# Kernel tuning notes

Hardware: AMD Instinct MI355X
Metric: run time of the kernel (lower is better)

Reference implementation:

```python
import jax, jax.numpy as jnp
import numpy as np

TAU = 0.2
LW = 0.5
EPS = 1e-12  # tf.math.l2_normalize epsilon


def _l2norm(x):
    ss = jnp.sum(x * x, axis=-1, keepdims=True)
    return x * jax.lax.rsqrt(jnp.maximum(ss, EPS))


def _global_head(f, W1, b1, W2, b2):
    g = jnp.mean(f, axis=(1, 2))            # GlobalAveragePooling2D -> [B, C]
    h = jax.nn.relu(g @ W1 + b1)
    return h @ W2 + b2                      # [B, 128]


def _dense_head(f, W1, b1, W2, b2):
    # 1x1 convs == per-pixel matmuls
    h = jax.nn.relu(jnp.einsum('bhwc,cd->bhwd', f, W1) + b1)
    return jnp.einsum('bhwd,de->bhwe', h, W2) + b2  # [B, H, W, 128]


def _info_nce(q, k):
    logits = (q @ k.T) / TAU                # [N, N]
    lse = jax.nn.logsumexp(logits, axis=-1)
    pos = jnp.diagonal(logits)
    return jnp.mean(lse - pos)


def setup_inputs() -> dict:
    key = jax.random.key(0)
    ks = jax.random.split(key, 10)
    B, H, W, C = 128, 7, 7, 2048
    Dh, De = 2048, 128
    s1 = 1.0 / np.sqrt(C)
    s2 = 1.0 / np.sqrt(Dh)
    inp = {
        'feat_q': jax.random.normal(ks[0], (B, H, W, C), jnp.float32),
        'feat_k': jax.random.normal(ks[1], (B, H, W, C), jnp.float32),
        'Wg1': jax.random.normal(ks[2], (C, Dh), jnp.float32) * s1,
        'bg1': jnp.zeros((Dh,), jnp.float32),
        'Wg2': jax.random.normal(ks[3], (Dh, De), jnp.float32) * s2,
        'bg2': jnp.zeros((De,), jnp.float32),
        'Wd1': jax.random.normal(ks[4], (C, Dh), jnp.float32) * s1,
        'bd1': jnp.zeros((Dh,), jnp.float32),
        'Wd2': jax.random.normal(ks[5], (Dh, De), jnp.float32) * s2,
        'bd2': jnp.zeros((De,), jnp.float32),
        'mWg1': jax.random.normal(ks[6], (C, Dh), jnp.float32) * s1,
        'mbg1': jnp.zeros((Dh,), jnp.float32),
        'mWg2': jax.random.normal(ks[7], (Dh, De), jnp.float32) * s2,
        'mbg2': jnp.zeros((De,), jnp.float32),
        'mWd1': jax.random.normal(ks[8], (C, Dh), jnp.float32) * s1,
        'mbd1': jnp.zeros((Dh,), jnp.float32),
        'mWd2': jax.random.normal(ks[9], (Dh, De), jnp.float32) * s2,
        'mbd2': jnp.zeros((De,), jnp.float32),
    }
    return inp


def reference(feat_q, feat_k, Wg1, bg1, Wg2, bg2, Wd1, bd1, Wd2, bd2,
              mWg1, mbg1, mWg2, mbg2, mWd1, mbd1, mWd2, mbd2):
    # query (student) branch
    q_g = _l2norm(_global_head(feat_q, Wg1, bg1, Wg2, bg2))      # [B, 128]
    q_d = _l2norm(_dense_head(feat_q, Wd1, bd1, Wd2, bd2))       # [B, H, W, 128]
    # key (momentum teacher) branch, stop-gradient as in train_step
    k_g = jax.lax.stop_gradient(_l2norm(_global_head(feat_k, mWg1, mbg1, mWg2, mbg2)))
    k_d = jax.lax.stop_gradient(_l2norm(_dense_head(feat_k, mWd1, mbd1, mWd2, mbd2)))

    l_g = _info_nce(q_g, k_g)

    B, H, W, De = q_d.shape
    f1 = q_d.reshape(B, H * W, De)
    f2 = k_d.reshape(B, H * W, De)
    sim = jnp.einsum('bnc,bmc->bnm', f1, f2)                     # [B, HW, HW]
    idx = jnp.argmax(sim, axis=-1)                               # [B, HW]
    matched = jnp.take_along_axis(f2, idx[..., None], axis=1)    # [B, HW, 128]

    l_d = _info_nce(f1.reshape(-1, De), matched.reshape(-1, De))
    total = (1.0 - LW) * l_g + LW * l_d
    return total
```

## Files before the change

kernel.cpp:

```cpp
#include <hip/hip_runtime.h>
#include <cstddef>

typedef __bf16 bf16x8 __attribute__((ext_vector_type(8)));
typedef float  f32x4  __attribute__((ext_vector_type(4)));
typedef unsigned short u16x8 __attribute__((ext_vector_type(8)));

__device__ __forceinline__ float b2f(unsigned short u) {
    union { unsigned int i; float f; } v; v.i = ((unsigned int)u) << 16; return v.f;
}
__device__ __forceinline__ unsigned short f2b(float f) {
    union { float f; unsigned int i; } v; v.f = f;
    unsigned int r = v.i + 0x7fffu + ((v.i >> 16) & 1u);
    return (unsigned short)(r >> 16);
}
__device__ __forceinline__ void gl_lds16(const void* g, void* l) {
    __builtin_amdgcn_global_load_lds((const __attribute__((address_space(1))) void*)g,
                                     (__attribute__((address_space(3))) void*)l,
                                     16, 0, 0);
}

__global__ __launch_bounds__(64) void detect_kernel(const unsigned short* __restrict__ feat,
                                                    int* __restrict__ flag) {
    __shared__ int cnt;
    if (threadIdx.x == 0) cnt = 0;
    __syncthreads();
    int c = 0;
    for (int i = threadIdx.x; i < 256; i += 64) {
        float v = b2f(feat[i]);
        if (fabsf(v) > 100.0f) ++c;
    }
    atomicAdd(&cnt, c);
    __syncthreads();
    if (threadIdx.x == 0) *flag = (cnt > 16) ? 1 : 0;
}

__global__ __launch_bounds__(256) void zero_kernel(float* __restrict__ p, int n4) {
    int i = blockIdx.x * 256 + threadIdx.x;
    const f32x4 z = {0.f, 0.f, 0.f, 0.f};
    if (i < n4) ((f32x4*)p)[i] = z;
}

__global__ __launch_bounds__(256) void convpool_kernel(const void* __restrict__ fq,
                                                       const void* __restrict__ fk,
                                                       unsigned short* __restrict__ FQ,
                                                       unsigned short* __restrict__ FK,
                                                       unsigned short* __restrict__ gq,
                                                       unsigned short* __restrict__ gk,
                                                       const int* __restrict__ flagp) {
    int fl = *flagp;
    int b = blockIdx.y;
    const void* src = blockIdx.z ? fk : fq;
    unsigned short* dst = blockIdx.z ? FK : FQ;
    unsigned short* g   = blockIdx.z ? gk : gq;
    int c0 = threadIdx.x * 8;
    float s[8];
    #pragma unroll
    for (int j = 0; j < 8; ++j) s[j] = 0.f;
    for (int p = 0; p < 49; ++p) {
        size_t idx = ((size_t)b * 49 + p) * 2048 + c0;
        u16x8 o;
        if (fl) {
            const float* sf = (const float*)src + idx;
            f32x4 v0 = *(const f32x4*)sf;
            f32x4 v1 = *(const f32x4*)(sf + 4);
            o[0]=f2b(v0[0]); o[1]=f2b(v0[1]); o[2]=f2b(v0[2]); o[3]=f2b(v0[3]);
            o[4]=f2b(v1[0]); o[5]=f2b(v1[1]); o[6]=f2b(v1[2]); o[7]=f2b(v1[3]);
            s[0]+=v0[0]; s[1]+=v0[1]; s[2]+=v0[2]; s[3]+=v0[3];
            s[4]+=v1[0]; s[5]+=v1[1]; s[6]+=v1[2]; s[7]+=v1[3];
        } else {
            o = *(const u16x8*)((const unsigned short*)src + idx);
            #pragma unroll
            for (int j = 0; j < 8; ++j) s[j] += b2f(o[j]);
        }
        *(u16x8*)(dst + idx) = o;
    }
    u16x8 gm;
    #pragma unroll
    for (int j = 0; j < 8; ++j) gm[j] = f2b(s[j] * (1.0f / 49.0f));
    *(u16x8*)(g + (size_t)b * 2048 + c0) = gm;
}

__global__ __launch_bounds__(256) void convert_kernel(const void* __restrict__ in,
                                                      unsigned short* __restrict__ out,
                                                      const int* __restrict__ flagp) {
    int fl = *flagp;
    size_t i = ((size_t)blockIdx.x * 256 + threadIdx.x) * 8;
    if (fl) {
        const float* inf = (const float*)in;
        f32x4 v0 = *(const f32x4*)(inf + i);
        f32x4 v1 = *(const f32x4*)(inf + i + 4);
        u16x8 o;
        o[0]=f2b(v0[0]); o[1]=f2b(v0[1]); o[2]=f2b(v0[2]); o[3]=f2b(v0[3]);
        o[4]=f2b(v1[0]); o[5]=f2b(v1[1]); o[6]=f2b(v1[2]); o[7]=f2b(v1[3]);
        *(u16x8*)(out + i) = o;
    } else {
        *(u16x8*)(out + i) = *(const u16x8*)((const unsigned short*)in + i);
    }
}

__global__ __launch_bounds__(256) void pool_kernel(const void* __restrict__ fq,
                                                   const void* __restrict__ fk,
                                                   unsigned short* __restrict__ gq,
                                                   unsigned short* __restrict__ gk,
                                                   const int* __restrict__ flagp) {
    int fl = *flagp;
    int c = blockIdx.x * 256 + threadIdx.x;
    int b = blockIdx.y;
    const void* src = blockIdx.z ? fk : fq;
    unsigned short* dst = blockIdx.z ? gk : gq;
    size_t base = (size_t)b * 49 * 2048 + c;
    float s = 0.f;
    if (fl) {
        const float* sf = (const float*)src;
        #pragma unroll
        for (int p = 0; p < 49; ++p) s += sf[base + (size_t)p * 2048];
    } else {
        const unsigned short* su = (const unsigned short*)src;
        #pragma unroll
        for (int p = 0; p < 49; ++p) s += b2f(su[base + (size_t)p * 2048]);
    }
    dst[(size_t)b * 2048 + c] = f2b(s * (1.0f / 49.0f));
}

__global__ __launch_bounds__(256) void transpose2v_kernel(
    const void* __restrict__ s0, const void* __restrict__ s1,
    unsigned short* __restrict__ d0, unsigned short* __restrict__ d1,
    int rows, int cols, const int* __restrict__ flagp) {
    int fl = *flagp;
    int z = blockIdx.z;
    const void* in = z ? s1 : s0;
    unsigned short* out = z ? d1 : d0;
    __shared__ unsigned short tile[64 * 72];
    int bx = blockIdx.x * 64, by = blockIdx.y * 64;
    int tr = threadIdx.x >> 3;
    int tc = (threadIdx.x & 7) * 8;
    #pragma unroll
    for (int h = 0; h < 2; ++h) {
        int r = tr + h * 32;
        if (fl) {
            const float* inf = (const float*)in + (size_t)(by + r) * cols + bx + tc;
            f32x4 v0 = *(const f32x4*)inf;
            f32x4 v1 = *(const f32x4*)(inf + 4);
            u16x8 o;
            o[0]=f2b(v0[0]); o[1]=f2b(v0[1]); o[2]=f2b(v0[2]); o[3]=f2b(v0[3]);
            o[4]=f2b(v1[0]); o[5]=f2b(v1[1]); o[6]=f2b(v1[2]); o[7]=f2b(v1[3]);
            *(u16x8*)(tile + r * 72 + tc) = o;
        } else {
            const unsigned short* inu = (const unsigned short*)in + (size_t)(by + r) * cols + bx + tc;
            *(u16x8*)(tile + r * 72 + tc) = *(const u16x8*)inu;
        }
    }
    __syncthreads();
    #pragma unroll
    for (int h = 0; h < 2; ++h) {
        int oc = tr + h * 32;
        u16x8 v;
        #pragma unroll
        for (int j = 0; j < 8; ++j) v[j] = tile[(tc + j) * 72 + oc];
        *(u16x8*)(out + (size_t)(bx + oc) * rows + by + tc) = v;
    }
}

__global__ __launch_bounds__(256) void transpose4v_kernel(
    const void* __restrict__ s0, const void* __restrict__ s1,
    const void* __restrict__ s2, const void* __restrict__ s3,
    unsigned short* __restrict__ d0, unsigned short* __restrict__ d1,
    unsigned short* __restrict__ d2, unsigned short* __restrict__ d3,
    int rows, int cols, const int* __restrict__ flagp) {
    int fl = *flagp;
    int z = blockIdx.z;
    const void* in = (z == 0) ? s0 : (z == 1) ? s1 : (z == 2) ? s2 : s3;
    unsigned short* out = (z == 0) ? d0 : (z == 1) ? d1 : (z == 2) ? d2 : d3;
    __shared__ unsigned short tile[64 * 72];
    int bx = blockIdx.x * 64, by = blockIdx.y * 64;
    int tr = threadIdx.x >> 3;
    int tc = (threadIdx.x & 7) * 8;
    #pragma unroll
    for (int h = 0; h < 2; ++h) {
        int r = tr + h * 32;
        if (fl) {
            const float* inf = (const float*)in + (size_t)(by + r) * cols + bx + tc;
            f32x4 v0 = *(const f32x4*)inf;
            f32x4 v1 = *(const f32x4*)(inf + 4);
            u16x8 o;
            o[0]=f2b(v0[0]); o[1]=f2b(v0[1]); o[2]=f2b(v0[2]); o[3]=f2b(v0[3]);
            o[4]=f2b(v1[0]); o[5]=f2b(v1[1]); o[6]=f2b(v1[2]); o[7]=f2b(v1[3]);
            *(u16x8*)(tile + r * 72 + tc) = o;
        } else {
            const unsigned short* inu = (const unsigned short*)in + (size_t)(by + r) * cols + bx + tc;
            *(u16x8*)(tile + r * 72 + tc) = *(const u16x8*)inu;
        }
    }
    __syncthreads();
    #pragma unroll
    for (int h = 0; h < 2; ++h) {
        int oc = tr + h * 32;
        u16x8 v;
        #pragma unroll
        for (int j = 0; j < 8; ++j) v[j] = tile[(tc + j) * 72 + oc];
        *(u16x8*)(out + (size_t)(bx + oc) * rows + by + tc) = v;
    }
}

__device__ __forceinline__ void mlp_body(
    const unsigned short* __restrict__ A, const unsigned short* __restrict__ Bt,
    const unsigned short* __restrict__ W2, const void* __restrict__ b1,
    float* __restrict__ outp, size_t m0, size_t n0, int fl)
{
    const int K = 2048;
    __shared__ unsigned short smem[8192 + 9216];
    unsigned short* As = smem;
    unsigned short* Bs = smem + 8192;
    unsigned short* Hs = smem + 8192;

    int tid  = threadIdx.x;
    int lane = tid & 63;
    int w    = tid >> 6;
    int wm = w & 1, wn = w >> 1;
    int quad = lane >> 4, l16 = lane & 15;
    int lrow = lane >> 3;
    int kc   = (lane & 7) ^ lrow;

    const unsigned short* gA[4];
    const unsigned short* gB[4];
    unsigned short* lA[4];
    unsigned short* lB[4];
    #pragma unroll
    for (int c = 0; c < 4; ++c) {
        int row = w * 32 + c * 8 + lrow;
        gA[c] = A  + (m0 + row) * (size_t)K + kc * 8;
        gB[c] = Bt + (n0 + row) * (size_t)K + kc * 8;
        lA[c] = As + w * 2048 + c * 512;
        lB[c] = Bs + w * 2048 + c * 512;
    }

    const f32x4 zero4 = {0.f, 0.f, 0.f, 0.f};
    f32x4 acc[4][4];
    #pragma unroll
    for (int i = 0; i < 4; ++i)
        #pragma unroll
        for (int j = 0; j < 4; ++j) acc[i][j] = zero4;

    int swz = l16 & 7;
    for (int kb = 0; kb < K / 64; ++kb) {
        __syncthreads();
        #pragma unroll
        for (int c = 0; c < 4; ++c) { gl_lds16(gA[c], lA[c]); gA[c] += 64; }
        #pragma unroll
        for (int c = 0; c < 4; ++c) { gl_lds16(gB[c], lB[c]); gB[c] += 64; }
        __syncthreads();
        #pragma unroll
        for (int k0 = 0; k0 < 64; k0 += 32) {
            bf16x8 af[4], bfr[4];
            #pragma unroll
            for (int mt = 0; mt < 4; ++mt) {
                int row = wm * 64 + mt * 16 + l16;
                int sc  = (((k0 >> 3) + quad) ^ swz) << 3;
                af[mt] = *(const bf16x8*)(As + row * 64 + sc);
            }
            #pragma unroll
            for (int nt = 0; nt < 4; ++nt) {
                int row = wn * 64 + nt * 16 + l16;
                int sc  = (((k0 >> 3) + quad) ^ swz) << 3;
                bfr[nt] = *(const bf16x8*)(Bs + row * 64 + sc);
            }
            #pragma unroll
            for (int mt = 0; mt < 4; ++mt)
                #pragma unroll
                for (int nt = 0; nt < 4; ++nt)
                    acc[mt][nt] = __builtin_amdgcn_mfma_f32_16x16x32_bf16(af[mt], bfr[nt], acc[mt][nt], 0, 0, 0);
        }
    }

    float b1v[4];
    #pragma unroll
    for (int nt = 0; nt < 4; ++nt) {
        int col = (int)n0 + wn * 64 + nt * 16 + l16;
        b1v[nt] = fl ? ((const float*)b1)[col] : b2f(((const unsigned short*)b1)[col]);
    }

    f32x4 acc2[4][4];
    #pragma unroll
    for (int i = 0; i < 4; ++i)
        #pragma unroll
        for (int j = 0; j < 4; ++j) acc2[i][j] = zero4;

    #pragma unroll
    for (int hf = 0; hf < 2; ++hf) {
        __syncthreads();
        if (wn == hf) {
            #pragma unroll
            for (int mt = 0; mt < 4; ++mt)
                #pragma unroll
                for (int nt = 0; nt < 4; ++nt)
                    #pragma unroll
                    for (int r = 0; r < 4; ++r) {
                        float v = fmaxf(acc[mt][nt][r] + b1v[nt], 0.f);
                        Hs[(wm * 64 + mt * 16 + quad * 4 + r) * 72 + nt * 16 + l16] = f2b(v);
                    }
        } else {
            #pragma unroll
            for (int c = 0; c < 8; ++c) {
                const unsigned short* g = W2 + (size_t)(wm * 64 + c * 8 + lrow) * 2048
                                          + n0 + hf * 64 + kc * 8;
                gl_lds16(g, As + wm * 4096 + c * 512);
            }
        }
        __syncthreads();
        #pragma unroll
        for (int k0 = 0; k0 < 64; k0 += 32) {
            bf16x8 ha[4], wb[4];
            #pragma unroll
            for (int mt = 0; mt < 4; ++mt)
                ha[mt] = *(const bf16x8*)(Hs + (wm * 64 + mt * 16 + l16) * 72 + k0 + quad * 8);
            #pragma unroll
            for (int et = 0; et < 4; ++et) {
                int row = wn * 64 + et * 16 + l16;
                int sc  = (((k0 >> 3) + quad) ^ swz) << 3;
                wb[et] = *(const bf16x8*)(As + row * 64 + sc);
            }
            #pragma unroll
            for (int mt = 0; mt < 4; ++mt)
                #pragma unroll
                for (int et = 0; et < 4; ++et)
                    acc2[mt][et] = __builtin_amdgcn_mfma_f32_16x16x32_bf16(ha[mt], wb[et], acc2[mt][et], 0, 0, 0);
        }
    }

    #pragma unroll
    for (int et = 0; et < 4; ++et) {
        int col = wn * 64 + et * 16 + l16;
        #pragma unroll
        for (int mt = 0; mt < 4; ++mt)
            #pragma unroll
            for (int r = 0; r < 4; ++r) {
                size_t row = m0 + wm * 64 + mt * 16 + quad * 4 + r;
                atomicAdd(&outp[row * 128 + col], acc2[mt][et][r]);
            }
    }
}

__global__ __launch_bounds__(256) void mlp_mega_kernel(
    const unsigned short* __restrict__ FQ, const unsigned short* __restrict__ FK,
    const unsigned short* __restrict__ gq, const unsigned short* __restrict__ gk,
    const unsigned short* __restrict__ WD1T, const unsigned short* __restrict__ MWD1T,
    const unsigned short* __restrict__ WG1T, const unsigned short* __restrict__ MWG1T,
    const unsigned short* __restrict__ W2dq, const unsigned short* __restrict__ W2dk,
    const unsigned short* __restrict__ W2gq, const unsigned short* __restrict__ W2gk,
    const void* __restrict__ bd1, const void* __restrict__ mbd1,
    const void* __restrict__ bg1, const void* __restrict__ mbg1,
    float* __restrict__ rawdq, float* __restrict__ rawdk,
    float* __restrict__ rawgq, float* __restrict__ rawgk,
    const int* __restrict__ flagp)
{
    int fl = *flagp;
    int z = blockIdx.z;
    int isg = (blockIdx.y == 49);
    const unsigned short *A, *Bt, *W2; const void* b1; float* outp;
    if (!isg) {
        A = z ? FK : FQ;  Bt = z ? MWD1T : WD1T;  W2 = z ? W2dk : W2dq;
        b1 = z ? mbd1 : bd1;  outp = z ? rawdk : rawdq;
    } else {
        A = z ? gk : gq;  Bt = z ? MWG1T : WG1T;  W2 = z ? W2gk : W2gq;
        b1 = z ? mbg1 : bg1;  outp = z ? rawgk : rawgq;
    }
    size_t m0 = isg ? 0 : (size_t)blockIdx.y * 128;
    size_t n0 = (size_t)blockIdx.x * 128;
    mlp_body(A, Bt, W2, b1, outp, m0, n0, fl);
}

__global__ __launch_bounds__(256) void mlp_kernel(
    const unsigned short* __restrict__ A0, const unsigned short* __restrict__ A1,
    const unsigned short* __restrict__ Bt0, const unsigned short* __restrict__ Bt1,
    const unsigned short* __restrict__ W20, const unsigned short* __restrict__ W21,
    const void* __restrict__ b10, const void* __restrict__ b11,
    float* __restrict__ out0, float* __restrict__ out1,
    const int* __restrict__ flagp)
{
    int fl = *flagp;
    int z  = blockIdx.z;
    mlp_body(z ? A1 : A0, z ? Bt1 : Bt0, z ? W21 : W20, z ? b11 : b10,
             z ? out1 : out0, (size_t)blockIdx.y * 128, (size_t)blockIdx.x * 128, fl);
}

__global__ __launch_bounds__(256) void simmatch_kernel(
    const float* __restrict__ rawdq, const float* __restrict__ rawdk,
    const void* __restrict__ bd2, const void* __restrict__ mbd2,
    unsigned short* __restrict__ qd, unsigned short* __restrict__ kd,
    unsigned short* __restrict__ matched, float* __restrict__ pos,
    const int* __restrict__ flagp) {
    int fl = *flagp;
    __shared__ float f1s[49 * 128];
    __shared__ float f2s[49 * 128];
    int b = blockIdx.x;
    int t = threadIdx.x;
    size_t base = (size_t)b * 49 * 128;

    int rr = t >> 2, jq = t & 3;
    if (rr < 49) {
        #pragma unroll
        for (int br = 0; br < 2; ++br) {
            const float* raw = br ? rawdk : rawdq;
            const void* bias = br ? mbd2 : bd2;
            unsigned short* outg = br ? kd : qd;
            float* fs = br ? f2s : f1s;
            size_t idx = base + (size_t)rr * 128 + jq * 32;
            float x[32];
            float ss = 0.f;
            #pragma unroll
            for (int c = 0; c < 32; ++c) {
                float bv = fl ? ((const float*)bias)[jq * 32 + c]
                              : b2f(((const unsigned short*)bias)[jq * 32 + c]);
                x[c] = raw[idx + c] + bv;
                ss += x[c] * x[c];
            }
            ss += __shfl_xor(ss, 1); ss += __shfl_xor(ss, 2);
            float rs = rsqrtf(fmaxf(ss, 1e-12f));
            #pragma unroll
            for (int c = 0; c < 32; ++c) {
                unsigned short us = f2b(x[c] * rs);
                outg[idx + c] = us;
                fs[rr * 128 + jq * 32 + c] = b2f(us);
            }
        }
    }
    __syncthreads();

    int i = t >> 2, q4 = t & 3;
    if (i < 49) {
        int mlo = q4 * 13;
        int mhi = mlo + 13; if (mhi > 49) mhi = 49;
        float best = -1e30f; int bi = 1 << 20;
        const f32x4* va = (const f32x4*)(f1s + i * 128);
        for (int m = mlo; m < mhi; ++m) {
            const f32x4* vb = (const f32x4*)(f2s + m * 128);
            float d = 0.f;
            #pragma unroll
            for (int j = 0; j < 32; ++j) {
                f32x4 a = va[j], bb = vb[j];
                d += a[0]*bb[0] + a[1]*bb[1] + a[2]*bb[2] + a[3]*bb[3];
            }
            if (d > best) { best = d; bi = m; }
        }
        #pragma unroll
        for (int off = 1; off < 4; off <<= 1) {
            float ov = __shfl_xor(best, off);
            int   oi = __shfl_xor(bi, off);
            if (ov > best || (ov == best && oi < bi)) { best = ov; bi = oi; }
        }
        if (q4 == 0) pos[b * 49 + i] = best * 5.0f;
        for (int j = q4 * 32; j < q4 * 32 + 32; ++j)
            matched[base + (size_t)i * 128 + j] = f2b(f2s[bi * 128 + j]);
    }
}

#define KS 136
__global__ __launch_bounds__(256) void lse_kernel(const unsigned short* __restrict__ qd,
                                                  const unsigned short* __restrict__ matched,
                                                  float* __restrict__ lsep) {
    __shared__ unsigned short As[128 * KS];
    __shared__ unsigned short Bs[64 * KS];
    __shared__ float rsum[128];
    int tid  = threadIdx.x;
    int lane = tid & 63, wave = tid >> 6;
    int wm = wave & 1, wn = wave >> 1;
    int quad = lane >> 4, l16 = lane & 15;
    size_t m0 = (size_t)blockIdx.x * 128;
    int z = blockIdx.y;

    #pragma unroll
    for (int i = 0; i < 8; ++i) {
        int l = tid + 256 * i;
        int row = l >> 4, ko = (l & 15) << 3;
        u16x8 v = *(const u16x8*)(qd + (m0 + row) * 128 + ko);
        *(u16x8*)(As + row * KS + ko) = v;
    }
    if (tid < 128) rsum[tid] = 0.f;

    float rs[4][4];
    #pragma unroll
    for (int mt = 0; mt < 4; ++mt)
        #pragma unroll
        for (int r = 0; r < 4; ++r) rs[mt][r] = 0.f;

    const f32x4 zero4 = {0.f, 0.f, 0.f, 0.f};
    int nlo = z * 896, nhi = nlo + 896;
    for (int n0 = nlo; n0 < nhi; n0 += 64) {
        __syncthreads();
        #pragma unroll
        for (int i = 0; i < 4; ++i) {
            int l = tid + 256 * i;
            int row = l >> 4, ko = (l & 15) << 3;
            u16x8 v = *(const u16x8*)(matched + (size_t)(n0 + row) * 128 + ko);
            *(u16x8*)(Bs + row * KS + ko) = v;
        }
        __syncthreads();
        f32x4 acc[4][2];
        #pragma unroll
        for (int mt = 0; mt < 4; ++mt) { acc[mt][0] = zero4; acc[mt][1] = zero4; }
        #pragma unroll
        for (int k0 = 0; k0 < 128; k0 += 32) {
            bf16x8 af[4], bfr[2];
            #pragma unroll
            for (int mt = 0; mt < 4; ++mt)
                af[mt] = *(const bf16x8*)(As + (wm * 64 + mt * 16 + l16) * KS + k0 + quad * 8);
            #pragma unroll
            for (int nt = 0; nt < 2; ++nt)
                bfr[nt] = *(const bf16x8*)(Bs + (wn * 32 + nt * 16 + l16) * KS + k0 + quad * 8);
            #pragma unroll
            for (int mt = 0; mt < 4; ++mt)
                #pragma unroll
                for (int nt = 0; nt < 2; ++nt)
                    acc[mt][nt] = __builtin_amdgcn_mfma_f32_16x16x32_bf16(af[mt], bfr[nt], acc[mt][nt], 0, 0, 0);
        }
        #pragma unroll
        for (int mt = 0; mt < 4; ++mt)
            #pragma unroll
            for (int r = 0; r < 4; ++r)
                rs[mt][r] += __expf(acc[mt][0][r] * 5.0f) + __expf(acc[mt][1][r] * 5.0f);
    }
    #pragma unroll
    for (int mt = 0; mt < 4; ++mt)
        #pragma unroll
        for (int r = 0; r < 4; ++r) {
            float v = rs[mt][r];
            v += __shfl_xor(v, 1); v += __shfl_xor(v, 2);
            v += __shfl_xor(v, 4); v += __shfl_xor(v, 8);
            if (l16 == 0) atomicAdd(&rsum[wm * 64 + mt * 16 + quad * 4 + r], v);
        }
    __syncthreads();
    if (tid < 128) lsep[(size_t)z * 6272 + m0 + tid] = rsum[tid];
}

__global__ __launch_bounds__(128) void lg_kernel(const float* __restrict__ rawgq,
                                                 const float* __restrict__ rawgk,
                                                 const void* __restrict__ bg2,
                                                 const void* __restrict__ mbg2,
                                                 float* __restrict__ lgrow,
                                                 const int* __restrict__ flagp) {
    int fl = *flagp;
    __shared__ float ksf[128 * 128];
    __shared__ float qsf[8 * 128];
    int t = threadIdx.x;
    int rbase = blockIdx.x * 8;
    {
        const float* rk = rawgk + (size_t)t * 128;
        float ss = 0.f;
        for (int c = 0; c < 128; ++c) {
            float bv = fl ? ((const float*)mbg2)[c] : b2f(((const unsigned short*)mbg2)[c]);
            float xx = rk[c] + bv;
            ss += xx * xx;
        }
        float rsv = rsqrtf(fmaxf(ss, 1e-12f));
        for (int c = 0; c < 128; ++c) {
            float bv = fl ? ((const float*)mbg2)[c] : b2f(((const unsigned short*)mbg2)[c]);
            ksf[t * 128 + c] = b2f(f2b((rk[c] + bv) * rsv));
        }
    }
    if (t < 8) {
        const float* rq = rawgq + (size_t)(rbase + t) * 128;
        float ss = 0.f;
        for (int c = 0; c < 128; ++c) {
            float bv = fl ? ((const float*)bg2)[c] : b2f(((const unsigned short*)bg2)[c]);
            float xx = rq[c] + bv;
            ss += xx * xx;
        }
        float rsv = rsqrtf(fmaxf(ss, 1e-12f));
        for (int c = 0; c < 128; ++c) {
            float bv = fl ? ((const float*)bg2)[c] : b2f(((const unsigned short*)bg2)[c]);
            qsf[t * 128 + c] = b2f(f2b((rq[c] + bv) * rsv));
        }
    }
    __syncthreads();
    int rl = t >> 4, jg = t & 15;
    int row = rbase + rl;
    float se = 0.f, diag = 0.f;
    for (int jj = 0; jj < 8; ++jj) {
        int j = jg * 8 + jj;
        float d = 0.f;
        #pragma unroll 8
        for (int c = 0; c < 128; ++c) d += qsf[rl * 128 + c] * ksf[j * 128 + c];
        d *= 5.0f;
        se += __expf(d);
        if (j == row) diag = d;
    }
    #pragma unroll
    for (int off = 1; off < 16; off <<= 1) { se += __shfl_xor(se, off); diag += __shfl_xor(diag, off); }
    if (jg == 0) lgrow[row] = logf(se) - diag;
}

__global__ __launch_bounds__(256) void final_kernel(const float* __restrict__ lsep,
                                                    const float* __restrict__ pos,
                                                    const float* __restrict__ lgrow,
                                                    unsigned int* __restrict__ out) {
    int t = threadIdx.x;
    float s = 0.f;
    for (int i = t; i < 6272; i += 256) {
        float se = 0.f;
        #pragma unroll
        for (int zz = 0; zz < 7; ++zz) se += lsep[zz * 6272 + i];
        s += logf(se) - pos[i];
    }
    float g = (t < 128) ? lgrow[t] : 0.f;
    #pragma unroll
    for (int off = 32; off >= 1; off >>= 1) { s += __shfl_xor(s, off); g += __shfl_xor(g, off); }
    __shared__ float p8[8];
    if ((t & 63) == 0) { p8[t >> 6] = s; p8[4 + (t >> 6)] = g; }
    __syncthreads();
    if (t == 0) {
        float ld  = (p8[0] + p8[1] + p8[2] + p8[3]) * (1.0f / 6272.0f);
        float lg  = (p8[4] + p8[5] + p8[6] + p8[7]) * (1.0f / 128.0f);
        float total = 0.5f * lg + 0.5f * ld;
        unsigned int L = f2b(total);
        union { float f; unsigned int u; } tb; tb.f = total;
        unsigned int base = (tb.u & 0xFFFF0000u) | L;
        unsigned int bu = base; float be = 1e30f;
        #pragma unroll
        for (int d = -1; d <= 1; ++d) {
            unsigned int c = base + ((unsigned int)d << 16);
            union { unsigned int u; float f; } cv; cv.u = c;
            float e = fabsf(cv.f - total);
            if (e < be) { be = e; bu = c; }
        }
        out[0] = bu;
    }
}

#define A_FQ     ((size_t)0)
#define A_FK     ((size_t)25690112)
#define A_WD1T   ((size_t)51380224)
#define A_MWD1T  ((size_t)59768832)
#define A_WG1T   ((size_t)68157440)
#define A_MWG1T  ((size_t)76546048)
#define A_W2DQ   ((size_t)84934656)
#define A_W2DK   ((size_t)85458944)
#define A_W2GQ   ((size_t)85983232)
#define A_W2GK   ((size_t)86507520)
#define A_RAWDQ  ((size_t)87031808)
#define A_RAWDK  ((size_t)90243072)
#define A_RAWGQ  ((size_t)93454336)
#define A_RAWGK  ((size_t)93519872)
#define A_GQ     ((size_t)93585408)
#define A_GK     ((size_t)94109696)
#define A_QD     ((size_t)94633984)
#define A_KD     ((size_t)96239616)
#define A_MT     ((size_t)97845248)
#define A_POS    ((size_t)99450880)
#define A_LSEP   ((size_t)99475968)
#define A_LGR    ((size_t)99651584)
#define A_FLAG   ((size_t)99652096)
#define A_NEED   ((size_t)99652608)

#define B_SLOTA  ((size_t)0)
#define B_QD     ((size_t)0)
#define B_KD     ((size_t)1605632)
#define B_MT     ((size_t)3211264)
#define B_SLOTB  ((size_t)8388608)
#define B_W2DQ   ((size_t)34078720)
#define B_W2DK   ((size_t)34603008)
#define B_W2GQ   ((size_t)35127296)
#define B_W2GK   ((size_t)35651584)
#define B_RAWDQ  ((size_t)36175872)
#define B_RAWDK  ((size_t)39387136)
#define B_RAWGQ  ((size_t)42598400)
#define B_RAWGK  ((size_t)42663936)
#define B_GQ     ((size_t)42729472)
#define B_GK     ((size_t)43253760)
#define B_POS    ((size_t)42729472)
#define B_LSEP   ((size_t)42754560)
#define B_LGR    ((size_t)42930176)
#define B_FLAG   ((size_t)42930688)

extern "C" void kernel_launch(void* const* d_in, const int* in_sizes, int n_in,
                              void* d_out, int out_size, void* d_ws, size_t ws_size,
                              hipStream_t stream) {
    (void)in_sizes; (void)n_in; (void)out_size;
    const void* feat_q = d_in[0];
    const void* feat_k = d_in[1];
    const void* Wg1 = d_in[2];  const void* bg1 = d_in[3];
    const void* Wg2 = d_in[4];  const void* bg2 = d_in[5];
    const void* Wd1 = d_in[6];  const void* bd1 = d_in[7];
    const void* Wd2 = d_in[8];  const void* bd2 = d_in[9];
    const void* mWg1 = d_in[10]; const void* mbg1 = d_in[11];
    const void* mWg2 = d_in[12]; const void* mbg2 = d_in[13];
    const void* mWd1 = d_in[14]; const void* mbd1 = d_in[15];
    const void* mWd2 = d_in[16]; const void* mbd2 = d_in[17];
    char* ws = (char*)d_ws;

    if (ws_size >= A_NEED) {
        unsigned short* FQ    = (unsigned short*)(ws + A_FQ);
        unsigned short* FK    = (unsigned short*)(ws + A_FK);
        unsigned short* WD1T  = (unsigned short*)(ws + A_WD1T);
        unsigned short* MWD1T = (unsigned short*)(ws + A_MWD1T);
        unsigned short* WG1T  = (unsigned short*)(ws + A_WG1T);
        unsigned short* MWG1T = (unsigned short*)(ws + A_MWG1T);
        unsigned short* W2dq  = (unsigned short*)(ws + A_W2DQ);
        unsigned short* W2dk  = (unsigned short*)(ws + A_W2DK);
        unsigned short* W2gq  = (unsigned short*)(ws + A_W2GQ);
        unsigned short* W2gk  = (unsigned short*)(ws + A_W2GK);
        float* rawdq = (float*)(ws + A_RAWDQ);
        float* rawdk = (float*)(ws + A_RAWDK);
        float* rawgq = (float*)(ws + A_RAWGQ);
        float* rawgk = (float*)(ws + A_RAWGK);
        unsigned short* gq = (unsigned short*)(ws + A_GQ);
        unsigned short* gk = (unsigned short*)(ws + A_GK);
        unsigned short* qd = (unsigned short*)(ws + A_QD);
        unsigned short* kd = (unsigned short*)(ws + A_KD);
        unsigned short* mt = (unsigned short*)(ws + A_MT);
        float* pos  = (float*)(ws + A_POS);
        float* lsep = (float*)(ws + A_LSEP);
        float* lgr  = (float*)(ws + A_LGR);
        int*   flag = (int*)(ws + A_FLAG);

        detect_kernel<<<1, 64, 0, stream>>>((const unsigned short*)feat_q, flag);
        convpool_kernel<<<dim3(1, 128, 2), 256, 0, stream>>>(feat_q, feat_k, FQ, FK, gq, gk, flag);
        transpose4v_kernel<<<dim3(32, 32, 4), 256, 0, stream>>>(
            Wd1, mWd1, Wg1, mWg1, WD1T, MWD1T, WG1T, MWG1T, 2048, 2048, flag);
        transpose4v_kernel<<<dim3(2, 32, 4), 256, 0, stream>>>(
            Wd2, mWd2, Wg2, mWg2, W2dq, W2dk, W2gq, W2gk, 2048, 128, flag);
        zero_kernel<<<1600, 256, 0, stream>>>(rawdq, 409600);
        mlp_mega_kernel<<<dim3(16, 50, 2), 256, 0, stream>>>(
            FQ, FK, gq, gk, WD1T, MWD1T, WG1T, MWG1T,
            W2dq, W2dk, W2gq, W2gk, bd1, mbd1, bg1, mbg1,
            rawdq, rawdk, rawgq, rawgk, flag);
        simmatch_kernel<<<128, 256, 0, stream>>>(rawdq, rawdk, bd2, mbd2, qd, kd, mt, pos, flag);
        lse_kernel<<<dim3(49, 7), 256, 0, stream>>>(qd, mt, lsep);
        lg_kernel<<<16, 128, 0, stream>>>(rawgq, rawgk, bg2, mbg2, lgr, flag);
        final_kernel<<<1, 256, 0, stream>>>(lsep, pos, lgr, (unsigned int*)d_out);
    } else {
        unsigned short* slotA = (unsigned short*)(ws + B_SLOTA);
        unsigned short* slotB = (unsigned short*)(ws + B_SLOTB);
        unsigned short* W2dq = (unsigned short*)(ws + B_W2DQ);
        unsigned short* W2dk = (unsigned short*)(ws + B_W2DK);
        unsigned short* W2gq = (unsigned short*)(ws + B_W2GQ);
        unsigned short* W2gk = (unsigned short*)(ws + B_W2GK);
        float* rawdq = (float*)(ws + B_RAWDQ);
        float* rawdk = (float*)(ws + B_RAWDK);
        float* rawgq = (float*)(ws + B_RAWGQ);
        float* rawgk = (float*)(ws + B_RAWGK);
        unsigned short* gq = (unsigned short*)(ws + B_GQ);
        unsigned short* gk = (unsigned short*)(ws + B_GK);
        unsigned short* qd = (unsigned short*)(ws + B_QD);
        unsigned short* kd = (unsigned short*)(ws + B_KD);
        unsigned short* mt = (unsigned short*)(ws + B_MT);
        float* pos  = (float*)(ws + B_POS);
        float* lsep = (float*)(ws + B_LSEP);
        float* lgr  = (float*)(ws + B_LGR);
        int*   flag = (int*)(ws + B_FLAG);

        detect_kernel<<<1, 64, 0, stream>>>((const unsigned short*)feat_q, flag);
        pool_kernel<<<dim3(8, 128, 2), 256, 0, stream>>>(feat_q, feat_k, gq, gk, flag);
        transpose2v_kernel<<<dim3(32, 32, 2), 256, 0, stream>>>(Wg1, mWg1, slotA, slotB, 2048, 2048, flag);
        transpose4v_kernel<<<dim3(2, 32, 4), 256, 0, stream>>>(
            Wd2, mWd2, Wg2, mWg2, W2dq, W2dk, W2gq, W2gk, 2048, 128, flag);
        zero_kernel<<<1600, 256, 0, stream>>>(rawdq, 409600);
        mlp_kernel<<<dim3(16, 1, 2), 256, 0, stream>>>(
            gq, gk, slotA, slotB, W2gq, W2gk, bg1, mbg1, rawgq, rawgk, flag);
        transpose2v_kernel<<<dim3(32, 32, 1), 256, 0, stream>>>(Wd1, Wd1, slotA, slotA, 2048, 2048, flag);
        convert_kernel<<<6272, 256, 0, stream>>>(feat_q, slotB, flag);
        mlp_kernel<<<dim3(16, 49, 1), 256, 0, stream>>>(
            slotB, slotB, slotA, slotA, W2dq, W2dq, bd1, bd1, rawdq, rawdq, flag);
        transpose2v_kernel<<<dim3(32, 32, 1), 256, 0, stream>>>(mWd1, mWd1, slotA, slotA, 2048, 2048, flag);
        convert_kernel<<<6272, 256, 0, stream>>>(feat_k, slotB, flag);
        mlp_kernel<<<dim3(16, 49, 1), 256, 0, stream>>>(
            slotB, slotB, slotA, slotA, W2dk, W2dk, mbd1, mbd1, rawdk, rawdk, flag);
        simmatch_kernel<<<128, 256, 0, stream>>>(rawdq, rawdk, bd2, mbd2, qd, kd, mt, pos, flag);
        lse_kernel<<<dim3(49, 7), 256, 0, stream>>>(qd, mt, lsep);
        lg_kernel<<<16, 128, 0, stream>>>(rawgq, rawgk, bg2, mbg2, lgr, flag);
        final_kernel<<<1, 256, 0, stream>>>(lsep, pos, lgr, (unsigned int*)d_out);
    }
}
```

Baseline: 571.6 us.

## Double-buffer MLP GEMM LDS tiles, add XCD block swizzle, widen convpool grid

The MLP GEMM main loop now uses two LDS buffers, so the global-to-LDS loads for the next K-slice are issued while MFMAs run on the current one. This halves the barriers per K step. The mlp kernels also remap block indices so that neighbouring tiles land on the same XCD, which should improve L2 reuse of the shared weight and activation panels. The convpool kernel is split across twice as many blocks with 4-wide vectors to add parallelism. In exchange, LDS use grows to 64KB per block, which may lower occupancy.

```diff
diff --git a/kernel.cpp b/kernel.cpp
--- a/kernel.cpp
+++ b/kernel.cpp
@@ -4,6 +4,7 @@
 typedef __bf16 bf16x8 __attribute__((ext_vector_type(8)));
 typedef float  f32x4  __attribute__((ext_vector_type(4)));
 typedef unsigned short u16x8 __attribute__((ext_vector_type(8)));
+typedef unsigned short u16x4 __attribute__((ext_vector_type(4)));
 
 __device__ __forceinline__ float b2f(unsigned short u) {
     union { unsigned int i; float f; } v; v.i = ((unsigned int)u) << 16; return v.f;
@@ -17,6 +18,19 @@
     __builtin_amdgcn_global_load_lds((const __attribute__((address_space(1))) void*)g,
                                      (__attribute__((address_space(3))) void*)l,
                                      16, 0, 0);
+}
+
+__device__ __forceinline__ void xcd_swizzle(int& bx, int& by, int& bz) {
+    unsigned int nx = gridDim.x, ny = gridDim.y;
+    unsigned int n = nx * ny * gridDim.z;
+    unsigned int lin = blockIdx.x + nx * (blockIdx.y + ny * blockIdx.z);
+    unsigned int q = n >> 3, r = n & 7u;
+    unsigned int xcd = lin & 7u, off = lin >> 3;
+    unsigned int s = (xcd < r) ? (xcd * (q + 1u) + off)
+                               : (r * (q + 1u) + (xcd - r) * q + off);
+    bx = (int)(s % nx); s /= nx;
+    by = (int)(s % ny);
+    bz = (int)(s / ny);
 }
 
 __global__ __launch_bounds__(64) void detect_kernel(const unsigned short* __restrict__ feat,
@@ -52,32 +66,28 @@
     const void* src = blockIdx.z ? fk : fq;
     unsigned short* dst = blockIdx.z ? FK : FQ;
     unsigned short* g   = blockIdx.z ? gk : gq;
-    int c0 = threadIdx.x * 8;
-    float s[8];
-    #pragma unroll
-    for (int j = 0; j < 8; ++j) s[j] = 0.f;
+    int c0 = blockIdx.x * 1024 + threadIdx.x * 4;
+    float s[4];
+    #pragma unroll
+    for (int j = 0; j < 4; ++j) s[j] = 0.f;
     for (int p = 0; p < 49; ++p) {
         size_t idx = ((size_t)b * 49 + p) * 2048 + c0;
-        u16x8 o;
+        u16x4 o;
         if (fl) {
-            const float* sf = (const float*)src + idx;
-            f32x4 v0 = *(const f32x4*)sf;
-            f32x4 v1 = *(const f32x4*)(sf + 4);
-            o[0]=f2b(v0[0]); o[1]=f2b(v0[1]); o[2]=f2b(v0[2]); o[3]=f2b(v0[3]);
-            o[4]=f2b(v1[0]); o[5]=f2b(v1[1]); o[6]=f2b(v1[2]); o[7]=f2b(v1[3]);
-            s[0]+=v0[0]; s[1]+=v0[1]; s[2]+=v0[2]; s[3]+=v0[3];
-            s[4]+=v1[0]; s[5]+=v1[1]; s[6]+=v1[2]; s[7]+=v1[3];
+            f32x4 v = *(const f32x4*)((const float*)src + idx);
+            o[0]=f2b(v[0]); o[1]=f2b(v[1]); o[2]=f2b(v[2]); o[3]=f2b(v[3]);
+            s[0]+=v[0]; s[1]+=v[1]; s[2]+=v[2]; s[3]+=v[3];
         } else {
-            o = *(const u16x8*)((const unsigned short*)src + idx);
-            #pragma unroll
-            for (int j = 0; j < 8; ++j) s[j] += b2f(o[j]);
-        }
-        *(u16x8*)(dst + idx) = o;
-    }
-    u16x8 gm;
-    #pragma unroll
-    for (int j = 0; j < 8; ++j) gm[j] = f2b(s[j] * (1.0f / 49.0f));
-    *(u16x8*)(g + (size_t)b * 2048 + c0) = gm;
+            o = *(const u16x4*)((const unsigned short*)src + idx);
+            #pragma unroll
+            for (int j = 0; j < 4; ++j) s[j] += b2f(o[j]);
+        }
+        *(u16x4*)(dst + idx) = o;
+    }
+    u16x4 gm;
+    #pragma unroll
+    for (int j = 0; j < 4; ++j) gm[j] = f2b(s[j] * (1.0f / 49.0f));
+    *(u16x4*)(g + (size_t)b * 2048 + c0) = gm;
 }
 
 __global__ __launch_bounds__(256) void convert_kernel(const void* __restrict__ in,
@@ -208,10 +218,13 @@
     float* __restrict__ outp, size_t m0, size_t n0, int fl)
 {
     const int K = 2048;
-    __shared__ unsigned short smem[8192 + 9216];
-    unsigned short* As = smem;
-    unsigned short* Bs = smem + 8192;
-    unsigned short* Hs = smem + 8192;
+    __shared__ unsigned short smem[32768];
+    unsigned short* As0 = smem;
+    unsigned short* Bs0 = smem + 8192;
+    unsigned short* As1 = smem + 16384;
+    unsigned short* Bs1 = smem + 24576;
+    unsigned short* W2s = smem;
+    unsigned short* Hs  = smem + 8192;
 
     int tid  = threadIdx.x;
     int lane = tid & 63;
@@ -223,15 +236,13 @@
 
     const unsigned short* gA[4];
     const unsigned short* gB[4];
-    unsigned short* lA[4];
-    unsigned short* lB[4];
+    int off[4];
     #pragma unroll
     for (int c = 0; c < 4; ++c) {
         int row = w * 32 + c * 8 + lrow;
         gA[c] = A  + (m0 + row) * (size_t)K + kc * 8;
         gB[c] = Bt + (n0 + row) * (size_t)K + kc * 8;
-        lA[c] = As + w * 2048 + c * 512;
-        lB[c] = Bs + w * 2048 + c * 512;
+        off[c] = w * 2048 + c * 512;
     }
 
     const f32x4 zero4 = {0.f, 0.f, 0.f, 0.f};
@@ -242,35 +253,51 @@
         for (int j = 0; j < 4; ++j) acc[i][j] = zero4;
 
     int swz = l16 & 7;
-    for (int kb = 0; kb < K / 64; ++kb) {
+
+#define STAGE(Ad, Bd) do { \
+    _Pragma("unroll") \
+    for (int c = 0; c < 4; ++c) { gl_lds16(gA[c], (Ad) + off[c]); gA[c] += 64; } \
+    _Pragma("unroll") \
+    for (int c = 0; c < 4; ++c) { gl_lds16(gB[c], (Bd) + off[c]); gB[c] += 64; } \
+} while (0)
+
+#define CSTEP(Asrc, Bsrc) do { \
+    _Pragma("unroll") \
+    for (int k0 = 0; k0 < 64; k0 += 32) { \
+        bf16x8 af[4], bfr[4]; \
+        _Pragma("unroll") \
+        for (int mt = 0; mt < 4; ++mt) { \
+            int row = wm * 64 + mt * 16 + l16; \
+            int sc  = (((k0 >> 3) + quad) ^ swz) << 3; \
+            af[mt] = *(const bf16x8*)((Asrc) + row * 64 + sc); \
+        } \
+        _Pragma("unroll") \
+        for (int nt = 0; nt < 4; ++nt) { \
+            int row = wn * 64 + nt * 16 + l16; \
+            int sc  = (((k0 >> 3) + quad) ^ swz) << 3; \
+            bfr[nt] = *(const bf16x8*)((Bsrc) + row * 64 + sc); \
+        } \
+        _Pragma("unroll") \
+        for (int mt = 0; mt < 4; ++mt) \
+            _Pragma("unroll") \
+            for (int nt = 0; nt < 4; ++nt) \
+                acc[mt][nt] = __builtin_amdgcn_mfma_f32_16x16x32_bf16(af[mt], bfr[nt], acc[mt][nt], 0, 0, 0); \
+    } \
+} while (0)
+
+    STAGE(As0, Bs0);
+    __syncthreads();
+    #pragma unroll 1
+    for (int kb2 = 0; kb2 < 16; ++kb2) {
+        STAGE(As1, Bs1);
+        CSTEP(As0, Bs0);
         __syncthreads();
-        #pragma unroll
-        for (int c = 0; c < 4; ++c) { gl_lds16(gA[c], lA[c]); gA[c] += 64; }
-        #pragma unroll
-        for (int c = 0; c < 4; ++c) { gl_lds16(gB[c], lB[c]); gB[c] += 64; }
+        if (kb2 < 15) STAGE(As0, Bs0);
+        CSTEP(As1, Bs1);
         __syncthreads();
-        #pragma unroll
-        for (int k0 = 0; k0 < 64; k0 += 32) {
-            bf16x8 af[4], bfr[4];
-            #pragma unroll
-            for (int mt = 0; mt < 4; ++mt) {
-                int row = wm * 64 + mt * 16 + l16;
-                int sc  = (((k0 >> 3) + quad) ^ swz) << 3;
-                af[mt] = *(const bf16x8*)(As + row * 64 + sc);
-            }
-            #pragma unroll
-            for (int nt = 0; nt < 4; ++nt) {
-                int row = wn * 64 + nt * 16 + l16;
-                int sc  = (((k0 >> 3) + quad) ^ swz) << 3;
-                bfr[nt] = *(const bf16x8*)(Bs + row * 64 + sc);
-            }
-            #pragma unroll
-            for (int mt = 0; mt < 4; ++mt)
-                #pragma unroll
-                for (int nt = 0; nt < 4; ++nt)
-                    acc[mt][nt] = __builtin_amdgcn_mfma_f32_16x16x32_bf16(af[mt], bfr[nt], acc[mt][nt], 0, 0, 0);
-        }
-    }
+    }
+#undef STAGE
+#undef CSTEP
 
     float b1v[4];
     #pragma unroll
@@ -303,7 +330,7 @@
             for (int c = 0; c < 8; ++c) {
                 const unsigned short* g = W2 + (size_t)(wm * 64 + c * 8 + lrow) * 2048
                                           + n0 + hf * 64 + kc * 8;
-                gl_lds16(g, As + wm * 4096 + c * 512);
+                gl_lds16(g, W2s + wm * 4096 + c * 512);
             }
         }
         __syncthreads();
@@ -317,7 +344,7 @@
             for (int et = 0; et < 4; ++et) {
                 int row = wn * 64 + et * 16 + l16;
                 int sc  = (((k0 >> 3) + quad) ^ swz) << 3;
-                wb[et] = *(const bf16x8*)(As + row * 64 + sc);
+                wb[et] = *(const bf16x8*)(W2s + row * 64 + sc);
             }
             #pragma unroll
             for (int mt = 0; mt < 4; ++mt)
@@ -354,8 +381,10 @@
     const int* __restrict__ flagp)
 {
     int fl = *flagp;
-    int z = blockIdx.z;
-    int isg = (blockIdx.y == 49);
+    int bx, by, bz;
+    xcd_swizzle(bx, by, bz);
+    int z = bz;
+    int isg = (by == 49);
     const unsigned short *A, *Bt, *W2; const void* b1; float* outp;
     if (!isg) {
         A = z ? FK : FQ;  Bt = z ? MWD1T : WD1T;  W2 = z ? W2dk : W2dq;
@@ -364,8 +393,8 @@
         A = z ? gk : gq;  Bt = z ? MWG1T : WG1T;  W2 = z ? W2gk : W2gq;
         b1 = z ? mbg1 : bg1;  outp = z ? rawgk : rawgq;
     }
-    size_t m0 = isg ? 0 : (size_t)blockIdx.y * 128;
-    size_t n0 = (size_t)blockIdx.x * 128;
+    size_t m0 = isg ? 0 : (size_t)by * 128;
+    size_t n0 = (size_t)bx * 128;
     mlp_body(A, Bt, W2, b1, outp, m0, n0, fl);
 }
 
@@ -378,9 +407,11 @@
     const int* __restrict__ flagp)
 {
     int fl = *flagp;
-    int z  = blockIdx.z;
+    int bx, by, bz;
+    xcd_swizzle(bx, by, bz);
+    int z  = bz;
     mlp_body(z ? A1 : A0, z ? Bt1 : Bt0, z ? W21 : W20, z ? b11 : b10,
-             z ? out1 : out0, (size_t)blockIdx.y * 128, (size_t)blockIdx.x * 128, fl);
+             z ? out1 : out0, (size_t)by * 128, (size_t)bx * 128, fl);
 }
 
 __global__ __launch_bounds__(256) void simmatch_kernel(
@@ -713,7 +744,7 @@
         int*   flag = (int*)(ws + A_FLAG);
 
         detect_kernel<<<1, 64, 0, stream>>>((const unsigned short*)feat_q, flag);
-        convpool_kernel<<<dim3(1, 128, 2), 256, 0, stream>>>(feat_q, feat_k, FQ, FK, gq, gk, flag);
+        convpool_kernel<<<dim3(2, 128, 2), 256, 0, stream>>>(feat_q, feat_k, FQ, FK, gq, gk, flag);
         transpose4v_kernel<<<dim3(32, 32, 4), 256, 0, stream>>>(
             Wd1, mWd1, Wg1, mWg1, WD1T, MWD1T, WG1T, MWG1T, 2048, 2048, flag);
         transpose4v_kernel<<<dim3(2, 32, 4), 256, 0, stream>>>(
```

Measured after the change: 546.1 us. -4.5%, faster.
